# Performance work log

Measured on AMD Instinct MI355X. Metric: run time of the kernel, lower is better.

The kernel has to match this reference:

```python
import jax, jax.numpy as jnp
import numpy as np

N = 50000      # num nodes
DIN = 256
DOUT = 256
E = 400000     # edges per sign
NEG_SLOPE = 0.2  # LeakyReLU(0.2)


def setup_inputs() -> dict:
    key = jax.random.key(0)
    ks = jax.random.split(key, 12)
    p = lambda k, shp: jax.random.normal(k, shp, jnp.float32) * 0.05
    return {
        "node_reps": jax.random.normal(ks[0], (N, DIN), jnp.float32),
        "adj_pos": jax.random.randint(ks[1], (2, E), 0, N, dtype=jnp.int32),
        "adj_neg": jax.random.randint(ks[2], (2, E), 0, N, dtype=jnp.int32),
        "basis": p(ks[3], (2, DIN, DOUT)),        # num_bases=num_relations=2
        "att": p(ks[4], (2, 2)),
        "mapping_func": p(ks[5], (1, 2 * DOUT)),
        "bias": p(ks[6], (1, DOUT)),
        "theta1": p(ks[7], (DOUT, DOUT)),          # HGNN_conv 1 linear weight
        "b1": jnp.zeros((DOUT,), jnp.float32),
        "theta2": p(ks[8], (DOUT, DOUT)),          # HGNN_conv 2 linear weight
        "b2": jnp.zeros((DOUT,), jnp.float32),
    }


def reference(node_reps, adj_pos, adj_neg, basis, att, mapping_func, bias,
              theta1, b1, theta2, b2):
    # basis-decomposed relation weights: Wr[r] = sum_b att[r,b] * basis[b]
    Wr = (att @ basis.reshape(2, -1)).reshape(2, DIN, DOUT)
    h_pos = node_reps @ Wr[0]
    h_neg = node_reps @ Wr[1]
    # HGNN_conv feature transforms (linear + bias)
    h_pos = h_pos @ theta1 + b1
    h_neg = h_neg @ theta2 + b2

    # edge attention score: mapping_func . concat(h[src], h[dst])
    w_src = mapping_func[0, :DOUT]
    w_dst = mapping_func[0, DOUT:]
    e_pos = h_pos[adj_pos[0]] @ w_src + h_pos[adj_pos[1]] @ w_dst  # [E]
    e_neg = h_neg[adj_neg[0]] @ w_src + h_neg[adj_neg[1]] @ w_dst  # [E]
    e_all = jnp.concatenate([e_pos, e_neg])                         # [2E]
    coeff = jax.nn.sigmoid(jnp.where(e_all > 0, e_all, NEG_SLOPE * e_all))

    # symmetric degree normalization over the union graph
    rows_all = jnp.concatenate([adj_pos[0], adj_neg[0]])
    cols_all = jnp.concatenate([adj_pos[1], adj_neg[1]])
    deg = jnp.sqrt(jax.ops.segment_sum(
        jnp.ones_like(coeff), rows_all, num_segments=N))            # [N]
    coeff = coeff / (deg[rows_all] * deg[cols_all])

    # sparse aggregation (SpecialSpmm): out[r] += coeff_e * h[c]
    h_agg_pos = jax.ops.segment_sum(
        coeff[:E, None] * h_pos[adj_pos[1]], adj_pos[0], num_segments=N)
    h_agg_neg = jax.ops.segment_sum(
        coeff[E:, None] * h_neg[adj_neg[1]], adj_neg[0], num_segments=N)

    output = h_agg_pos - h_agg_neg + bias
    return (output, h_agg_pos, h_agg_neg)
```

## Files before the change

### kernel.cpp

```cpp
#include <hip/hip_runtime.h>

#define N_NODES 50000
#define NEDGE   400000
#define SB      512
#define NSB     ((N_NODES + SB - 1) / SB)
#define H8SCALE 128.0f

typedef __bf16 bf16x8 __attribute__((ext_vector_type(8)));
typedef float  f32x4  __attribute__((ext_vector_type(4)));
typedef float  f32x2  __attribute__((ext_vector_type(2)));
typedef unsigned short u16x8 __attribute__((ext_vector_type(8)));
typedef int    i32x2  __attribute__((ext_vector_type(2)));

#define GLDS16(gp, lp) \
  __builtin_amdgcn_global_load_lds((const __attribute__((address_space(1))) void*)(gp), \
                                   (__attribute__((address_space(3))) void*)(lp), 16, 0, 0)

static __device__ __forceinline__ unsigned short f2bf(float f) {
  unsigned u = __float_as_uint(f);
  unsigned r = (u + 0x7fffu + ((u >> 16) & 1u)) >> 16;
  return (unsigned short)r;
}
static __device__ __forceinline__ float bf2f(unsigned short v) {
  return __uint_as_float((unsigned)v << 16);
}

__global__ __launch_bounds__(256) void fused0_kernel(
    const float* __restrict__ basis, const float* __restrict__ att,
    const float* __restrict__ theta1, const float* __restrict__ theta2,
    const float* __restrict__ bias1, const float* __restrict__ bias2,
    unsigned short* __restrict__ Wt, float* __restrict__ biasvec,
    const float* __restrict__ node, unsigned short* __restrict__ A16,
    const int* __restrict__ adjp, const int* __restrict__ adjn,
    int* __restrict__ cntp, int* __restrict__ cntn) {
  const int b = blockIdx.x;
  if (b < 512) {
    const int r = b >> 8, k = b & 255;
    const int n = threadIdx.x;
    const float a0 = att[r * 2 + 0], a1 = att[r * 2 + 1];
    const float* th = (r == 0) ? theta1 : theta2;
    float acc = 0.f;
    for (int j = 0; j < 256; ++j) {
      const float wr = a0 * basis[k * 256 + j] + a1 * basis[65536 + k * 256 + j];
      acc += wr * th[j * 256 + n];
    }
    Wt[(size_t)(r * 256 + n) * 256 + k] = f2bf(acc);
    if (k == 0) biasvec[r * 256 + n] = (r == 0) ? bias1[n] : bias2[n];
  } else if (b < 2560) {
    const long total = (long)N_NODES * 256 / 4;
    long idx = (long)(b - 512) * 256 + threadIdx.x;
    const long stride = 2048L * 256;
    for (; idx < total; idx += stride) {
      const f32x4 v = __builtin_nontemporal_load(&((const f32x4*)node)[idx]);
      ushort4 o;
      o.x = f2bf(v.x); o.y = f2bf(v.y); o.z = f2bf(v.z); o.w = f2bf(v.w);
      ((ushort4*)A16)[idx] = o;
    }
  } else {
    const int g = (b - 2560) * 256 + threadIdx.x;
    if (g < NEDGE) atomicAdd(&cntp[adjp[g]], 1);
    else if (g < 2 * NEDGE) atomicAdd(&cntn[adjn[g - NEDGE]], 1);
  }
}

__global__ __launch_bounds__(256) void gemm_kernel(
    const unsigned short* __restrict__ A,
    const unsigned short* __restrict__ Wt,
    const float* __restrict__ biasvec,
    const float* __restrict__ mapping,
    unsigned char* __restrict__ H8,
    float* __restrict__ sdbuf) {
  __shared__ unsigned short smem[128 * 136];
  unsigned short* sA = smem;
  unsigned short* sB = smem + 8192;
  const int tid = threadIdx.x;
  const int wave = tid >> 6, lane = tid & 63;
  const int wm = wave >> 1, wn = wave & 1;
  const int m0 = blockIdx.y * 128;
  const int n0 = blockIdx.x * 128;

  f32x4 acc[4][4];
#pragma unroll
  for (int a = 0; a < 4; ++a)
#pragma unroll
    for (int b = 0; b < 4; ++b) acc[a][b] = (f32x4){0.f, 0.f, 0.f, 0.f};

  const int srow = lane >> 3;
  const int skel = ((lane & 7) ^ srow) << 3;

  for (int ks = 0; ks < 4; ++ks) {
    const int kg = ks * 64 + skel;
#pragma unroll
    for (int c = 0; c < 4; ++c) {
      const int chunk = wave * 4 + c;
      const int row = chunk * 8 + srow;
      int rowg = m0 + row;
      rowg = rowg < N_NODES ? rowg : N_NODES - 1;
      GLDS16(A + (size_t)rowg * 256 + kg, sA + chunk * 512);
      GLDS16(Wt + (size_t)(n0 + row) * 256 + kg, sB + chunk * 512);
    }
    __syncthreads();
#pragma unroll
    for (int kk = 0; kk < 2; ++kk) {
      const int kb = (kk * 32 + ((lane >> 4) << 3)) << 1;
      bf16x8 af[4], bfr[4];
#pragma unroll
      for (int m16 = 0; m16 < 4; ++m16) {
        const int row = wm * 64 + m16 * 16 + (lane & 15);
        af[m16] = *(const bf16x8*)((const char*)sA + row * 128 + (kb ^ ((row & 7) << 4)));
      }
#pragma unroll
      for (int n16 = 0; n16 < 4; ++n16) {
        const int col = wn * 64 + n16 * 16 + (lane & 15);
        bfr[n16] = *(const bf16x8*)((const char*)sB + col * 128 + (kb ^ ((col & 7) << 4)));
      }
#pragma unroll
      for (int m16 = 0; m16 < 4; ++m16)
#pragma unroll
        for (int n16 = 0; n16 < 4; ++n16)
          acc[m16][n16] = __builtin_amdgcn_mfma_f32_16x16x32_bf16(af[m16], bfr[n16], acc[m16][n16], 0, 0, 0);
    }
    __syncthreads();
  }

  const bool sgn = (n0 >= 256);
  const int nb = (sgn ? (n0 - 256) : n0) >> 7;
  const int slice = nb * 2 + wn;
  float* __restrict__ sS = sdbuf + ((size_t)((sgn ? 2 : 0) + 0) * 4 + slice) * N_NODES;
  float* __restrict__ sD = sdbuf + ((size_t)((sgn ? 2 : 0) + 1) * 4 + slice) * N_NODES;
  float bv[4], wsv[4], wdv[4];
#pragma unroll
  for (int n16 = 0; n16 < 4; ++n16) {
    const int colg = n0 + wn * 64 + n16 * 16 + (lane & 15);
    bv[n16] = biasvec[colg];
    const int cm = colg & 255;
    wsv[n16] = mapping[cm];
    wdv[n16] = mapping[256 + cm];
  }
#pragma unroll
  for (int m16 = 0; m16 < 4; ++m16) {
    const int rowb = wm * 64 + m16 * 16 + ((lane >> 4) << 2);
#pragma unroll
    for (int j = 0; j < 4; ++j) {
      const int rowl = rowb + j;
      float vs = 0.f, vd = 0.f;
#pragma unroll
      for (int n16 = 0; n16 < 4; ++n16) {
        const float v = acc[m16][n16][j] + bv[n16];
        const int coll = wn * 64 + n16 * 16 + (lane & 15);
        smem[rowl * 136 + coll] = f2bf(v);
        vs += v * wsv[n16];
        vd += v * wdv[n16];
      }
#pragma unroll
      for (int off = 1; off < 16; off <<= 1) { vs += __shfl_xor(vs, off); vd += __shfl_xor(vd, off); }
      const int rowg = m0 + rowl;
      if ((lane & 15) == 0 && rowg < N_NODES) { sS[rowg] = vs; sD[rowg] = vd; }
    }
  }
  __syncthreads();
#pragma unroll
  for (int it = 0; it < 8; ++it) {
    const int row = it * 16 + (tid >> 4);
    const int c8 = (tid & 15) * 8;
    const int rowg = m0 + row;
    if (rowg < N_NODES) {
      const u16x8 v = *(const u16x8*)(smem + row * 136 + c8);
      float f[8];
#pragma unroll
      for (int q = 0; q < 8; ++q) f[q] = bf2f((unsigned short)v[q]) * H8SCALE;
      int w0 = __builtin_amdgcn_cvt_pk_fp8_f32(f[0], f[1], 0, false);
      w0     = __builtin_amdgcn_cvt_pk_fp8_f32(f[2], f[3], w0, true);
      int w1 = __builtin_amdgcn_cvt_pk_fp8_f32(f[4], f[5], 0, false);
      w1     = __builtin_amdgcn_cvt_pk_fp8_f32(f[6], f[7], w1, true);
      i32x2 o; o.x = w0; o.y = w1;
      *(i32x2*)(&H8[(size_t)rowg * 512 + n0 + c8]) = o;
    }
  }
}

__global__ __launch_bounds__(SB) void scan1_kernel(const int* __restrict__ cntp,
                                                   const int* __restrict__ cntn,
                                                   int* __restrict__ bsp, int* __restrict__ bsn) {
  __shared__ int lp[SB / 64], ln[SB / 64];
  const int i = blockIdx.x * SB + threadIdx.x;
  int vp = (i < N_NODES) ? cntp[i] : 0;
  int vn = (i < N_NODES) ? cntn[i] : 0;
#pragma unroll
  for (int off = 1; off < 64; off <<= 1) { vp += __shfl_xor(vp, off); vn += __shfl_xor(vn, off); }
  const int wave = threadIdx.x >> 6, lane = threadIdx.x & 63;
  if (lane == 0) { lp[wave] = vp; ln[wave] = vn; }
  __syncthreads();
  if (threadIdx.x == 0) {
    int ap = 0, an = 0;
#pragma unroll
    for (int w = 0; w < SB / 64; ++w) { ap += lp[w]; an += ln[w]; }
    bsp[blockIdx.x] = ap; bsn[blockIdx.x] = an;
  }
}

__global__ void scan2_kernel(int* __restrict__ bsp, int* __restrict__ bsn,
                             int* __restrict__ rsp, int* __restrict__ rsn) {
  __shared__ int sp_[128], sn_[128];
  const int t = threadIdx.x;
  sp_[t] = (t < NSB) ? bsp[t] : 0;
  sn_[t] = (t < NSB) ? bsn[t] : 0;
  __syncthreads();
  for (int off = 1; off < 128; off <<= 1) {
    const int ap = (t >= off) ? sp_[t - off] : 0;
    const int an = (t >= off) ? sn_[t - off] : 0;
    __syncthreads();
    sp_[t] += ap; sn_[t] += an;
    __syncthreads();
  }
  if (t < NSB) { bsp[t] = (t == 0) ? 0 : sp_[t - 1]; bsn[t] = (t == 0) ? 0 : sn_[t - 1]; }
  if (t == 127) { rsp[N_NODES] = sp_[127]; rsn[N_NODES] = sn_[127]; }
}

__global__ __launch_bounds__(SB) void scan3_kernel(const int* __restrict__ cntp,
                                                   const int* __restrict__ cntn,
                                                   const int* __restrict__ bsp,
                                                   const int* __restrict__ bsn,
                                                   const float* __restrict__ sdbuf,
                                                   int* __restrict__ rsp, int* __restrict__ rsn,
                                                   int* __restrict__ curp, int* __restrict__ curn,
                                                   f32x4* __restrict__ nip, f32x4* __restrict__ nin) {
  __shared__ int sp_[SB], sn_[SB];
  const int t = threadIdx.x;
  const int i = blockIdx.x * SB + t;
  const int cp = (i < N_NODES) ? cntp[i] : 0;
  const int cn = (i < N_NODES) ? cntn[i] : 0;
  sp_[t] = cp; sn_[t] = cn;
  __syncthreads();
  for (int off = 1; off < SB; off <<= 1) {
    const int ap = (t >= off) ? sp_[t - off] : 0;
    const int an = (t >= off) ? sn_[t - off] : 0;
    __syncthreads();
    sp_[t] += ap; sn_[t] += an;
    __syncthreads();
  }
  if (i < N_NODES) {
    const int rp = bsp[blockIdx.x] + sp_[t] - cp;
    const int rn = bsn[blockIdx.x] + sn_[t] - cn;
    rsp[i] = rp; curp[i] = rp;
    rsn[i] = rn; curn[i] = rn;
    const float rdeg = 1.f / sqrtf((float)(cp + cn));
    float sp4 = 0.f, dp4 = 0.f, sn4 = 0.f, dn4 = 0.f;
#pragma unroll
    for (int sl = 0; sl < 4; ++sl) {
      sp4 += sdbuf[(size_t)(0 * 4 + sl) * N_NODES + i];
      dp4 += sdbuf[(size_t)(1 * 4 + sl) * N_NODES + i];
      sn4 += sdbuf[(size_t)(2 * 4 + sl) * N_NODES + i];
      dn4 += sdbuf[(size_t)(3 * 4 + sl) * N_NODES + i];
    }
    nip[i] = (f32x4){sp4, dp4, rdeg, 0.f};
    nin[i] = (f32x4){sn4, dn4, rdeg, 0.f};
  }
}

__global__ void scatter_kernel(const int* __restrict__ adjp, const int* __restrict__ adjn,
                               const f32x4* __restrict__ nip, const f32x4* __restrict__ nin,
                               int* __restrict__ curp, int* __restrict__ curn,
                               i32x2* __restrict__ ecp, i32x2* __restrict__ ecn) {
  const int g = blockIdx.x * blockDim.x + threadIdx.x;
  if (g >= 2 * NEDGE) return;
  const bool neg = (g >= NEDGE);
  const int e2 = neg ? g - NEDGE : g;
  const int* __restrict__ adj = neg ? adjn : adjp;
  const f32x4* __restrict__ ni = neg ? nin : nip;
  int* __restrict__ cur = neg ? curn : curp;
  i32x2* __restrict__ ec = neg ? ecn : ecp;
  const int src = adj[e2], dst = adj[NEDGE + e2];
  const f32x4 a = ni[src], b = ni[dst];
  const float e = a.x + b.y;
  const float l = e > 0.f ? e : 0.2f * e;
  const float c = (1.f / (1.f + expf(-l))) * a.z * b.z * (1.0f / H8SCALE);
  const int p = atomicAdd(&cur[src], 1);
  i32x2 w; w.x = dst; w.y = __float_as_int(c);
  ec[p] = w;
}

__global__ __launch_bounds__(256) void agg_kernel(
    const unsigned char* __restrict__ H8,
    const int* __restrict__ rsp, const i32x2* __restrict__ ecp,
    const int* __restrict__ rsn, const i32x2* __restrict__ ecn,
    const float* __restrict__ bias, float* __restrict__ out) {
  __shared__ f32x4 sneg[2][64];
  const int wave = threadIdx.x >> 6, lane = threadIdx.x & 63;
  const int r = wave >> 1;
  const int sign = wave & 1;
  const int i = blockIdx.x * 2 + r;
  const int* __restrict__ rs  = sign ? rsn : rsp;
  const i32x2* __restrict__ ec = sign ? ecn : ecp;
  const unsigned char* __restrict__ Hb = H8 + sign * 256 + (size_t)lane * 4;
  const int beg = rs[i], end = rs[i + 1];
  f32x4 a0 = {0,0,0,0}, a1 = {0,0,0,0}, a2 = {0,0,0,0}, a3 = {0,0,0,0};
  for (int chunk = beg; chunk < end; chunk += 64) {
    const int m = (end - chunk < 64) ? end - chunk : 64;
    i32x2 ev = {0, 0};
    if (lane < m) ev = __builtin_nontemporal_load(&ec[chunk + lane]);
    const int   cv = ev.x;
    const float fv = __int_as_float(ev.y);
    int k = 0;
    for (; k + 4 <= m; k += 4) {
      const int   c0 = __shfl(cv, k),     c1 = __shfl(cv, k + 1);
      const int   c2 = __shfl(cv, k + 2), c3 = __shfl(cv, k + 3);
      const float f0 = __shfl(fv, k),     f1 = __shfl(fv, k + 1);
      const float f2 = __shfl(fv, k + 2), f3 = __shfl(fv, k + 3);
      const unsigned w0 = *(const unsigned*)(Hb + (size_t)c0 * 512);
      const unsigned w1 = *(const unsigned*)(Hb + (size_t)c1 * 512);
      const unsigned w2 = *(const unsigned*)(Hb + (size_t)c2 * 512);
      const unsigned w3 = *(const unsigned*)(Hb + (size_t)c3 * 512);
      const f32x2 l0 = __builtin_amdgcn_cvt_pk_f32_fp8(w0, false), h0 = __builtin_amdgcn_cvt_pk_f32_fp8(w0, true);
      const f32x2 l1 = __builtin_amdgcn_cvt_pk_f32_fp8(w1, false), h1 = __builtin_amdgcn_cvt_pk_f32_fp8(w1, true);
      const f32x2 l2 = __builtin_amdgcn_cvt_pk_f32_fp8(w2, false), h2 = __builtin_amdgcn_cvt_pk_f32_fp8(w2, true);
      const f32x2 l3 = __builtin_amdgcn_cvt_pk_f32_fp8(w3, false), h3 = __builtin_amdgcn_cvt_pk_f32_fp8(w3, true);
      a0.x += f0 * l0.x; a0.y += f0 * l0.y; a0.z += f0 * h0.x; a0.w += f0 * h0.y;
      a1.x += f1 * l1.x; a1.y += f1 * l1.y; a1.z += f1 * h1.x; a1.w += f1 * h1.y;
      a2.x += f2 * l2.x; a2.y += f2 * l2.y; a2.z += f2 * h2.x; a2.w += f2 * h2.y;
      a3.x += f3 * l3.x; a3.y += f3 * l3.y; a3.z += f3 * h3.x; a3.w += f3 * h3.y;
    }
    for (; k < m; ++k) {
      const int   c0 = __shfl(cv, k);
      const float f0 = __shfl(fv, k);
      const unsigned w0 = *(const unsigned*)(Hb + (size_t)c0 * 512);
      const f32x2 l0 = __builtin_amdgcn_cvt_pk_f32_fp8(w0, false), h0 = __builtin_amdgcn_cvt_pk_f32_fp8(w0, true);
      a0.x += f0 * l0.x; a0.y += f0 * l0.y; a0.z += f0 * h0.x; a0.w += f0 * h0.y;
    }
  }
  f32x4 a = (a0 + a1) + (a2 + a3);
  if (sign) sneg[r][lane] = a;
  __syncthreads();
  if (sign) {
    __builtin_nontemporal_store(a, ((f32x4*)(out + (size_t)2 * N_NODES * 256)) + (size_t)i * 64 + lane);
  } else {
    const f32x4 an = sneg[r][lane];
    const f32x4 bv = ((const f32x4*)bias)[lane];
    const f32x4 o = a - an + bv;
    __builtin_nontemporal_store(o, ((f32x4*)out) + (size_t)i * 64 + lane);
    __builtin_nontemporal_store(a, ((f32x4*)(out + (size_t)N_NODES * 256)) + (size_t)i * 64 + lane);
  }
}

extern "C" void kernel_launch(void* const* d_in, const int* in_sizes, int n_in,
                              void* d_out, int out_size, void* d_ws, size_t ws_size,
                              hipStream_t stream) {
  const float* node    = (const float*)d_in[0];
  const int*   adjp    = (const int*)d_in[1];
  const int*   adjn    = (const int*)d_in[2];
  const float* basis   = (const float*)d_in[3];
  const float* att     = (const float*)d_in[4];
  const float* mapping = (const float*)d_in[5];
  const float* bias    = (const float*)d_in[6];
  const float* theta1  = (const float*)d_in[7];
  const float* b1      = (const float*)d_in[8];
  const float* theta2  = (const float*)d_in[9];
  const float* b2      = (const float*)d_in[10];
  float* out = (float*)d_out;

  size_t off = 0;
  char* wsb = (char*)d_ws;
  auto alloc = [&](size_t bytes) -> char* {
    char* p = wsb + off;
    off = (off + bytes + 255) & ~(size_t)255;
    return p;
  };
  unsigned short* A16 = (unsigned short*)alloc((size_t)N_NODES * 256 * 2);
  unsigned char*  H8  = (unsigned char*)alloc((size_t)N_NODES * 512);
  unsigned short* Wt  = (unsigned short*)alloc(512 * 256 * 2);
  float* biasvec = (float*)alloc(512 * 4);
  float* sdbuf = (float*)alloc((size_t)16 * N_NODES * 4);
  f32x4* nip = (f32x4*)alloc((size_t)N_NODES * 16);
  f32x4* nin = (f32x4*)alloc((size_t)N_NODES * 16);
  int* cnt2 = (int*)alloc((size_t)2 * N_NODES * 4);
  int* cntp = cnt2, *cntn = cnt2 + N_NODES;
  int* cur2 = (int*)alloc((size_t)2 * N_NODES * 4);
  int* curp = cur2, *curn = cur2 + N_NODES;
  int* rsp = (int*)alloc((N_NODES + 1) * 4);
  int* rsn = (int*)alloc((N_NODES + 1) * 4);
  int* bsp = (int*)alloc(NSB * 4);
  int* bsn = (int*)alloc(NSB * 4);
  i32x2* ecp = (i32x2*)alloc((size_t)NEDGE * 8);
  i32x2* ecn = (i32x2*)alloc((size_t)NEDGE * 8);

  (void)hipMemsetAsync(cnt2, 0, (size_t)2 * N_NODES * 4, stream);

  fused0_kernel<<<512 + 2048 + (2 * NEDGE) / 256, 256, 0, stream>>>(
      basis, att, theta1, theta2, b1, b2, Wt, biasvec, node, A16, adjp, adjn, cntp, cntn);
  gemm_kernel<<<dim3(4, 391), 256, 0, stream>>>(A16, Wt, biasvec, mapping, H8, sdbuf);
  scan1_kernel<<<NSB, SB, 0, stream>>>(cntp, cntn, bsp, bsn);
  scan2_kernel<<<1, 128, 0, stream>>>(bsp, bsn, rsp, rsn);
  scan3_kernel<<<NSB, SB, 0, stream>>>(cntp, cntn, bsp, bsn, sdbuf, rsp, rsn, curp, curn, nip, nin);
  scatter_kernel<<<(2 * NEDGE) / 256, 256, 0, stream>>>(adjp, adjn, nip, nin, curp, curn, ecp, ecn);
  agg_kernel<<<N_NODES / 2, 256, 0, stream>>>(H8, rsp, ecp, rsn, ecn, bias, out);
}
```

Before: 214.5 us.

## Fuse fp32-to-bf16 node conversion into GEMM and widen N tile to 256

```diff
diff --git a/kernel.cpp b/kernel.cpp
--- a/kernel.cpp
+++ b/kernel.cpp
@@ -21,8 +21,8 @@
   unsigned r = (u + 0x7fffu + ((u >> 16) & 1u)) >> 16;
   return (unsigned short)r;
 }
-static __device__ __forceinline__ float bf2f(unsigned short v) {
-  return __uint_as_float((unsigned)v << 16);
+static __device__ __forceinline__ unsigned char f2fp8(float f) {
+  return (unsigned char)(__builtin_amdgcn_cvt_pk_fp8_f32(f, f, 0, false) & 0xff);
 }
 
 __global__ __launch_bounds__(256) void fused0_kernel(
@@ -30,7 +30,6 @@
     const float* __restrict__ theta1, const float* __restrict__ theta2,
     const float* __restrict__ bias1, const float* __restrict__ bias2,
     unsigned short* __restrict__ Wt, float* __restrict__ biasvec,
-    const float* __restrict__ node, unsigned short* __restrict__ A16,
     const int* __restrict__ adjp, const int* __restrict__ adjn,
     int* __restrict__ cntp, int* __restrict__ cntn) {
   const int b = blockIdx.x;
@@ -46,92 +45,96 @@
     }
     Wt[(size_t)(r * 256 + n) * 256 + k] = f2bf(acc);
     if (k == 0) biasvec[r * 256 + n] = (r == 0) ? bias1[n] : bias2[n];
-  } else if (b < 2560) {
-    const long total = (long)N_NODES * 256 / 4;
-    long idx = (long)(b - 512) * 256 + threadIdx.x;
-    const long stride = 2048L * 256;
-    for (; idx < total; idx += stride) {
-      const f32x4 v = __builtin_nontemporal_load(&((const f32x4*)node)[idx]);
-      ushort4 o;
-      o.x = f2bf(v.x); o.y = f2bf(v.y); o.z = f2bf(v.z); o.w = f2bf(v.w);
-      ((ushort4*)A16)[idx] = o;
-    }
   } else {
-    const int g = (b - 2560) * 256 + threadIdx.x;
+    const int g = (b - 512) * 256 + threadIdx.x;
     if (g < NEDGE) atomicAdd(&cntp[adjp[g]], 1);
-    else if (g < 2 * NEDGE) atomicAdd(&cntn[adjn[g - NEDGE]], 1);
+    else           atomicAdd(&cntn[adjn[g - NEDGE]], 1);
   }
 }
 
 __global__ __launch_bounds__(256) void gemm_kernel(
-    const unsigned short* __restrict__ A,
+    const float* __restrict__ Af,
     const unsigned short* __restrict__ Wt,
     const float* __restrict__ biasvec,
     const float* __restrict__ mapping,
     unsigned char* __restrict__ H8,
     float* __restrict__ sdbuf) {
-  __shared__ unsigned short smem[128 * 136];
+  __shared__ unsigned short smem[24576];
   unsigned short* sA = smem;
   unsigned short* sB = smem + 8192;
   const int tid = threadIdx.x;
   const int wave = tid >> 6, lane = tid & 63;
   const int wm = wave >> 1, wn = wave & 1;
+  const int sgn = blockIdx.x;
   const int m0 = blockIdx.y * 128;
-  const int n0 = blockIdx.x * 128;
-
-  f32x4 acc[4][4];
+  const int n0 = sgn * 256;
+
+  f32x4 acc[4][8];
 #pragma unroll
   for (int a = 0; a < 4; ++a)
 #pragma unroll
-    for (int b = 0; b < 4; ++b) acc[a][b] = (f32x4){0.f, 0.f, 0.f, 0.f};
+    for (int b = 0; b < 8; ++b) acc[a][b] = (f32x4){0.f, 0.f, 0.f, 0.f};
 
   const int srow = lane >> 3;
   const int skel = ((lane & 7) ^ srow) << 3;
+  const int arow = tid >> 1;
+  const int akh  = (tid & 1) * 32;
+  int arowg = m0 + arow;
+  arowg = arowg < N_NODES ? arowg : N_NODES - 1;
+  const f32x4* asrc = (const f32x4*)(Af + (size_t)arowg * 256 + akh);
+  const int aswz = (arow & 7) << 4;
 
   for (int ks = 0; ks < 4; ++ks) {
     const int kg = ks * 64 + skel;
 #pragma unroll
-    for (int c = 0; c < 4; ++c) {
-      const int chunk = wave * 4 + c;
-      const int row = chunk * 8 + srow;
-      int rowg = m0 + row;
-      rowg = rowg < N_NODES ? rowg : N_NODES - 1;
-      GLDS16(A + (size_t)rowg * 256 + kg, sA + chunk * 512);
-      GLDS16(Wt + (size_t)(n0 + row) * 256 + kg, sB + chunk * 512);
+    for (int c = 0; c < 8; ++c) {
+      const int chunk = wave * 8 + c;
+      const int brow = chunk * 8 + srow;
+      GLDS16(Wt + (size_t)(n0 + brow) * 256 + kg, sB + chunk * 512);
+    }
+    {
+      const f32x4* src = asrc + ks * 16;
+#pragma unroll
+      for (int c = 0; c < 4; ++c) {
+        const f32x4 v0 = src[c * 2], v1 = src[c * 2 + 1];
+        u16x8 hv;
+        hv[0] = f2bf(v0.x); hv[1] = f2bf(v0.y); hv[2] = f2bf(v0.z); hv[3] = f2bf(v0.w);
+        hv[4] = f2bf(v1.x); hv[5] = f2bf(v1.y); hv[6] = f2bf(v1.z); hv[7] = f2bf(v1.w);
+        const int boff = arow * 128 + ((akh * 2 + c * 16) ^ aswz);
+        *(u16x8*)((char*)sA + boff) = hv;
+      }
     }
     __syncthreads();
 #pragma unroll
     for (int kk = 0; kk < 2; ++kk) {
       const int kb = (kk * 32 + ((lane >> 4) << 3)) << 1;
-      bf16x8 af[4], bfr[4];
+      bf16x8 af[4], bfr[8];
 #pragma unroll
       for (int m16 = 0; m16 < 4; ++m16) {
         const int row = wm * 64 + m16 * 16 + (lane & 15);
         af[m16] = *(const bf16x8*)((const char*)sA + row * 128 + (kb ^ ((row & 7) << 4)));
       }
 #pragma unroll
-      for (int n16 = 0; n16 < 4; ++n16) {
-        const int col = wn * 64 + n16 * 16 + (lane & 15);
+      for (int n16 = 0; n16 < 8; ++n16) {
+        const int col = wn * 128 + n16 * 16 + (lane & 15);
         bfr[n16] = *(const bf16x8*)((const char*)sB + col * 128 + (kb ^ ((col & 7) << 4)));
       }
 #pragma unroll
       for (int m16 = 0; m16 < 4; ++m16)
 #pragma unroll
-        for (int n16 = 0; n16 < 4; ++n16)
+        for (int n16 = 0; n16 < 8; ++n16)
           acc[m16][n16] = __builtin_amdgcn_mfma_f32_16x16x32_bf16(af[m16], bfr[n16], acc[m16][n16], 0, 0, 0);
     }
     __syncthreads();
   }
 
-  const bool sgn = (n0 >= 256);
-  const int nb = (sgn ? (n0 - 256) : n0) >> 7;
-  const int slice = nb * 2 + wn;
-  float* __restrict__ sS = sdbuf + ((size_t)((sgn ? 2 : 0) + 0) * 4 + slice) * N_NODES;
-  float* __restrict__ sD = sdbuf + ((size_t)((sgn ? 2 : 0) + 1) * 4 + slice) * N_NODES;
-  float bv[4], wsv[4], wdv[4];
-#pragma unroll
-  for (int n16 = 0; n16 < 4; ++n16) {
-    const int colg = n0 + wn * 64 + n16 * 16 + (lane & 15);
+  unsigned char* smem8 = (unsigned char*)smem;
+  float* __restrict__ sS = sdbuf + ((size_t)((sgn * 2 + 0) * 2 + wn)) * N_NODES;
+  float* __restrict__ sD = sdbuf + ((size_t)((sgn * 2 + 1) * 2 + wn)) * N_NODES;
+  float bv[8], wsv[8], wdv[8];
+#pragma unroll
+  for (int n16 = 0; n16 < 8; ++n16) {
+    const int colg = n0 + wn * 128 + n16 * 16 + (lane & 15);
     bv[n16] = biasvec[colg];
     const int cm = colg & 255;
     wsv[n16] = mapping[cm];
@@ -145,10 +148,10 @@
       const int rowl = rowb + j;
       float vs = 0.f, vd = 0.f;
 #pragma unroll
-      for (int n16 = 0; n16 < 4; ++n16) {
+      for (int n16 = 0; n16 < 8; ++n16) {
         const float v = acc[m16][n16][j] + bv[n16];
-        const int coll = wn * 64 + n16 * 16 + (lane & 15);
-        smem[rowl * 136 + coll] = f2bf(v);
+        const int coll = wn * 128 + n16 * 16 + (lane & 15);
+        smem8[rowl * 272 + coll] = f2fp8(v * H8SCALE);
         vs += v * wsv[n16];
         vd += v * wdv[n16];
       }
@@ -159,22 +162,14 @@
     }
   }
   __syncthreads();
-#pragma unroll
-  for (int it = 0; it < 8; ++it) {
-    const int row = it * 16 + (tid >> 4);
-    const int c8 = (tid & 15) * 8;
+  {
+    const int row = tid >> 1, half = tid & 1;
     const int rowg = m0 + row;
     if (rowg < N_NODES) {
-      const u16x8 v = *(const u16x8*)(smem + row * 136 + c8);
-      float f[8];
-#pragma unroll
-      for (int q = 0; q < 8; ++q) f[q] = bf2f((unsigned short)v[q]) * H8SCALE;
-      int w0 = __builtin_amdgcn_cvt_pk_fp8_f32(f[0], f[1], 0, false);
-      w0     = __builtin_amdgcn_cvt_pk_fp8_f32(f[2], f[3], w0, true);
-      int w1 = __builtin_amdgcn_cvt_pk_fp8_f32(f[4], f[5], 0, false);
-      w1     = __builtin_amdgcn_cvt_pk_fp8_f32(f[6], f[7], w1, true);
-      i32x2 o; o.x = w0; o.y = w1;
-      *(i32x2*)(&H8[(size_t)rowg * 512 + n0 + c8]) = o;
+      const f32x4* s = (const f32x4*)(smem8 + row * 272 + half * 128);
+      f32x4* d = (f32x4*)(H8 + (size_t)rowg * 512 + n0 + half * 128);
+#pragma unroll
+      for (int c = 0; c < 8; ++c) d[c] = s[c];
     }
   }
 }
@@ -245,14 +240,10 @@
     rsp[i] = rp; curp[i] = rp;
     rsn[i] = rn; curn[i] = rn;
     const float rdeg = 1.f / sqrtf((float)(cp + cn));
-    float sp4 = 0.f, dp4 = 0.f, sn4 = 0.f, dn4 = 0.f;
-#pragma unroll
-    for (int sl = 0; sl < 4; ++sl) {
-      sp4 += sdbuf[(size_t)(0 * 4 + sl) * N_NODES + i];
-      dp4 += sdbuf[(size_t)(1 * 4 + sl) * N_NODES + i];
-      sn4 += sdbuf[(size_t)(2 * 4 + sl) * N_NODES + i];
-      dn4 += sdbuf[(size_t)(3 * 4 + sl) * N_NODES + i];
-    }
+    const float sp4 = sdbuf[(size_t)0 * N_NODES + i] + sdbuf[(size_t)1 * N_NODES + i];
+    const float dp4 = sdbuf[(size_t)2 * N_NODES + i] + sdbuf[(size_t)3 * N_NODES + i];
+    const float sn4 = sdbuf[(size_t)4 * N_NODES + i] + sdbuf[(size_t)5 * N_NODES + i];
+    const float dn4 = sdbuf[(size_t)6 * N_NODES + i] + sdbuf[(size_t)7 * N_NODES + i];
     nip[i] = (f32x4){sp4, dp4, rdeg, 0.f};
     nin[i] = (f32x4){sn4, dn4, rdeg, 0.f};
   }
@@ -295,6 +286,16 @@
   const unsigned char* __restrict__ Hb = H8 + sign * 256 + (size_t)lane * 4;
   const int beg = rs[i], end = rs[i + 1];
   f32x4 a0 = {0,0,0,0}, a1 = {0,0,0,0}, a2 = {0,0,0,0}, a3 = {0,0,0,0};
+  f32x4 a4 = {0,0,0,0}, a5 = {0,0,0,0}, a6 = {0,0,0,0}, a7 = {0,0,0,0};
+#define GSTEP(ACC, KOFF)                                                              \
+  {                                                                                   \
+    const int   c_ = __shfl(cv, k + (KOFF));                                          \
+    const float f_ = __shfl(fv, k + (KOFF));                                          \
+    const unsigned w_ = *(const unsigned*)(Hb + (size_t)c_ * 512);                    \
+    const f32x2 lo_ = __builtin_amdgcn_cvt_pk_f32_fp8(w_, false);                     \
+    const f32x2 hi_ = __builtin_amdgcn_cvt_pk_f32_fp8(w_, true);                      \
+    ACC.x += f_ * lo_.x; ACC.y += f_ * lo_.y; ACC.z += f_ * hi_.x; ACC.w += f_ * hi_.y; \
+  }
   for (int chunk = beg; chunk < end; chunk += 64) {
     const int m = (end - chunk < 64) ? end - chunk : 64;
     i32x2 ev = {0, 0};
@@ -302,33 +303,14 @@
     const int   cv = ev.x;
     const float fv = __int_as_float(ev.y);
     int k = 0;
-    for (; k + 4 <= m; k += 4) {
-      const int   c0 = __shfl(cv, k),     c1 = __shfl(cv, k + 1);
-      const int   c2 = __shfl(cv, k + 2), c3 = __shfl(cv, k + 3);
-      const float f0 = __shfl(fv, k),     f1 = __shfl(fv, k + 1);
-      const float f2 = __shfl(fv, k + 2), f3 = __shfl(fv, k + 3);
-      const unsigned w0 = *(const unsigned*)(Hb + (size_t)c0 * 512);
-      const unsigned w1 = *(const unsigned*)(Hb + (size_t)c1 * 512);
-      const unsigned w2 = *(const unsigned*)(Hb + (size_t)c2 * 512);
-      const unsigned w3 = *(const unsigned*)(Hb + (size_t)c3 * 512);
-      const f32x2 l0 = __builtin_amdgcn_cvt_pk_f32_fp8(w0, false), h0 = __builtin_amdgcn_cvt_pk_f32_fp8(w0, true);
-      const f32x2 l1 = __builtin_amdgcn_cvt_pk_f32_fp8(w1, false), h1 = __builtin_amdgcn_cvt_pk_f32_fp8(w1, true);
-      const f32x2 l2 = __builtin_amdgcn_cvt_pk_f32_fp8(w2, false), h2 = __builtin_amdgcn_cvt_pk_f32_fp8(w2, true);
-      const f32x2 l3 = __builtin_amdgcn_cvt_pk_f32_fp8(w3, false), h3 = __builtin_amdgcn_cvt_pk_f32_fp8(w3, true);
-      a0.x += f0 * l0.x; a0.y += f0 * l0.y; a0.z += f0 * h0.x; a0.w += f0 * h0.y;
-      a1.x += f1 * l1.x; a1.y += f1 * l1.y; a1.z += f1 * h1.x; a1.w += f1 * h1.y;
-      a2.x += f2 * l2.x; a2.y += f2 * l2.y; a2.z += f2 * h2.x; a2.w += f2 * h2.y;
-      a3.x += f3 * l3.x; a3.y += f3 * l3.y; a3.z += f3 * h3.x; a3.w += f3 * h3.y;
-    }
-    for (; k < m; ++k) {
-      const int   c0 = __shfl(cv, k);
-      const float f0 = __shfl(fv, k);
-      const unsigned w0 = *(const unsigned*)(Hb + (size_t)c0 * 512);
-      const f32x2 l0 = __builtin_amdgcn_cvt_pk_f32_fp8(w0, false), h0 = __builtin_amdgcn_cvt_pk_f32_fp8(w0, true);
-      a0.x += f0 * l0.x; a0.y += f0 * l0.y; a0.z += f0 * h0.x; a0.w += f0 * h0.y;
-    }
-  }
-  f32x4 a = (a0 + a1) + (a2 + a3);
+    for (; k + 8 <= m; k += 8) {
+      GSTEP(a0, 0) GSTEP(a1, 1) GSTEP(a2, 2) GSTEP(a3, 3)
+      GSTEP(a4, 4) GSTEP(a5, 5) GSTEP(a6, 6) GSTEP(a7, 7)
+    }
+    for (; k < m; ++k) GSTEP(a0, 0)
+  }
+#undef GSTEP
+  f32x4 a = ((a0 + a1) + (a2 + a3)) + ((a4 + a5) + (a6 + a7));
   if (sign) sneg[r][lane] = a;
   __syncthreads();
   if (sign) {
@@ -365,11 +347,10 @@
     off = (off + bytes + 255) & ~(size_t)255;
     return p;
   };
-  unsigned short* A16 = (unsigned short*)alloc((size_t)N_NODES * 256 * 2);
   unsigned char*  H8  = (unsigned char*)alloc((size_t)N_NODES * 512);
   unsigned short* Wt  = (unsigned short*)alloc(512 * 256 * 2);
   float* biasvec = (float*)alloc(512 * 4);
-  float* sdbuf = (float*)alloc((size_t)16 * N_NODES * 4);
+  float* sdbuf = (float*)alloc((size_t)8 * N_NODES * 4);
   f32x4* nip = (f32x4*)alloc((size_t)N_NODES * 16);
   f32x4* nin = (f32x4*)alloc((size_t)N_NODES * 16);
   int* cnt2 = (int*)alloc((size_t)2 * N_NODES * 4);
@@ -385,9 +366,9 @@
 
   (void)hipMemsetAsync(cnt2, 0, (size_t)2 * N_NODES * 4, stream);
 
-  fused0_kernel<<<512 + 2048 + (2 * NEDGE) / 256, 256, 0, stream>>>(
-      basis, att, theta1, theta2, b1, b2, Wt, biasvec, node, A16, adjp, adjn, cntp, cntn);
-  gemm_kernel<<<dim3(4, 391), 256, 0, stream>>>(A16, Wt, biasvec, mapping, H8, sdbuf);
+  fused0_kernel<<<512 + (2 * NEDGE) / 256, 256, 0, stream>>>(
+      basis, att, theta1, theta2, b1, b2, Wt, biasvec, adjp, adjn, cntp, cntn);
+  gemm_kernel<<<dim3(2, 391), 256, 0, stream>>>(node, Wt, biasvec, mapping, H8, sdbuf);
   scan1_kernel<<<NSB, SB, 0, stream>>>(cntp, cntn, bsp, bsn);
   scan2_kernel<<<1, 128, 0, stream>>>(bsp, bsn, rsp, rsn);
   scan3_kernel<<<NSB, SB, 0, stream>>>(cntp, cntn, bsp, bsn, sdbuf, rsp, rsn, curp, curn, nip, nin);
```

Result: slower. 270.4 us (+26.0%).

## Map 16-lane groups per edge with 16-byte fp8 row loads in aggregation

Applied to the files above, without the earlier changes.

```diff
diff --git a/kernel.cpp b/kernel.cpp
--- a/kernel.cpp
+++ b/kernel.cpp
@@ -11,6 +11,7 @@
 typedef float  f32x2  __attribute__((ext_vector_type(2)));
 typedef unsigned short u16x8 __attribute__((ext_vector_type(8)));
 typedef int    i32x2  __attribute__((ext_vector_type(2)));
+typedef unsigned int u32x4 __attribute__((ext_vector_type(4)));
 
 #define GLDS16(gp, lp) \
   __builtin_amdgcn_global_load_lds((const __attribute__((address_space(1))) void*)(gp), \
@@ -23,6 +24,12 @@
 }
 static __device__ __forceinline__ float bf2f(unsigned short v) {
   return __uint_as_float((unsigned)v << 16);
+}
+static __device__ __forceinline__ f32x4 shflxor4(f32x4 v, int m) {
+  f32x4 r;
+  r.x = __shfl_xor(v.x, m); r.y = __shfl_xor(v.y, m);
+  r.z = __shfl_xor(v.z, m); r.w = __shfl_xor(v.w, m);
+  return r;
 }
 
 __global__ __launch_bounds__(256) void fused0_kernel(
@@ -285,60 +292,63 @@
     const int* __restrict__ rsp, const i32x2* __restrict__ ecp,
     const int* __restrict__ rsn, const i32x2* __restrict__ ecn,
     const float* __restrict__ bias, float* __restrict__ out) {
-  __shared__ f32x4 sneg[2][64];
+  __shared__ float sneg[2][256];
   const int wave = threadIdx.x >> 6, lane = threadIdx.x & 63;
   const int r = wave >> 1;
   const int sign = wave & 1;
   const int i = blockIdx.x * 2 + r;
   const int* __restrict__ rs  = sign ? rsn : rsp;
   const i32x2* __restrict__ ec = sign ? ecn : ecp;
-  const unsigned char* __restrict__ Hb = H8 + sign * 256 + (size_t)lane * 4;
+  const int g16 = lane >> 4;
+  const int l16 = lane & 15;
+  const unsigned char* __restrict__ Hb = H8 + sign * 256 + l16 * 16;
   const int beg = rs[i], end = rs[i + 1];
-  f32x4 a0 = {0,0,0,0}, a1 = {0,0,0,0}, a2 = {0,0,0,0}, a3 = {0,0,0,0};
+  f32x4 A0 = {0,0,0,0}, A1 = {0,0,0,0}, A2 = {0,0,0,0}, A3 = {0,0,0,0};
+#define DECW(W, ACC)                                                                  \
+  {                                                                                   \
+    const f32x2 lo_ = __builtin_amdgcn_cvt_pk_f32_fp8((W), false);                    \
+    const f32x2 hi_ = __builtin_amdgcn_cvt_pk_f32_fp8((W), true);                     \
+    ACC.x += f_ * lo_.x; ACC.y += f_ * lo_.y; ACC.z += f_ * hi_.x; ACC.w += f_ * hi_.y; \
+  }
   for (int chunk = beg; chunk < end; chunk += 64) {
     const int m = (end - chunk < 64) ? end - chunk : 64;
     i32x2 ev = {0, 0};
     if (lane < m) ev = __builtin_nontemporal_load(&ec[chunk + lane]);
     const int   cv = ev.x;
     const float fv = __int_as_float(ev.y);
-    int k = 0;
-    for (; k + 4 <= m; k += 4) {
-      const int   c0 = __shfl(cv, k),     c1 = __shfl(cv, k + 1);
-      const int   c2 = __shfl(cv, k + 2), c3 = __shfl(cv, k + 3);
-      const float f0 = __shfl(fv, k),     f1 = __shfl(fv, k + 1);
-      const float f2 = __shfl(fv, k + 2), f3 = __shfl(fv, k + 3);
-      const unsigned w0 = *(const unsigned*)(Hb + (size_t)c0 * 512);
-      const unsigned w1 = *(const unsigned*)(Hb + (size_t)c1 * 512);
-      const unsigned w2 = *(const unsigned*)(Hb + (size_t)c2 * 512);
-      const unsigned w3 = *(const unsigned*)(Hb + (size_t)c3 * 512);
-      const f32x2 l0 = __builtin_amdgcn_cvt_pk_f32_fp8(w0, false), h0 = __builtin_amdgcn_cvt_pk_f32_fp8(w0, true);
-      const f32x2 l1 = __builtin_amdgcn_cvt_pk_f32_fp8(w1, false), h1 = __builtin_amdgcn_cvt_pk_f32_fp8(w1, true);
-      const f32x2 l2 = __builtin_amdgcn_cvt_pk_f32_fp8(w2, false), h2 = __builtin_amdgcn_cvt_pk_f32_fp8(w2, true);
-      const f32x2 l3 = __builtin_amdgcn_cvt_pk_f32_fp8(w3, false), h3 = __builtin_amdgcn_cvt_pk_f32_fp8(w3, true);
-      a0.x += f0 * l0.x; a0.y += f0 * l0.y; a0.z += f0 * h0.x; a0.w += f0 * h0.y;
-      a1.x += f1 * l1.x; a1.y += f1 * l1.y; a1.z += f1 * h1.x; a1.w += f1 * h1.y;
-      a2.x += f2 * l2.x; a2.y += f2 * l2.y; a2.z += f2 * h2.x; a2.w += f2 * h2.y;
-      a3.x += f3 * l3.x; a3.y += f3 * l3.y; a3.z += f3 * h3.x; a3.w += f3 * h3.y;
-    }
-    for (; k < m; ++k) {
-      const int   c0 = __shfl(cv, k);
-      const float f0 = __shfl(fv, k);
-      const unsigned w0 = *(const unsigned*)(Hb + (size_t)c0 * 512);
-      const f32x2 l0 = __builtin_amdgcn_cvt_pk_f32_fp8(w0, false), h0 = __builtin_amdgcn_cvt_pk_f32_fp8(w0, true);
-      a0.x += f0 * l0.x; a0.y += f0 * l0.y; a0.z += f0 * h0.x; a0.w += f0 * h0.y;
-    }
-  }
-  f32x4 a = (a0 + a1) + (a2 + a3);
-  if (sign) sneg[r][lane] = a;
+    for (int k = 0; k < m; k += 4) {
+      const int e = k + g16;
+      const int   c_ = __shfl(cv, e);
+      const float f_ = __shfl(fv, e);
+      const u32x4 w = *(const u32x4*)(Hb + (size_t)c_ * 512);
+      DECW(w[0], A0) DECW(w[1], A1) DECW(w[2], A2) DECW(w[3], A3)
+    }
+  }
+#undef DECW
+  A0 += shflxor4(A0, 16); A1 += shflxor4(A1, 16); A2 += shflxor4(A2, 16); A3 += shflxor4(A3, 16);
+  A0 += shflxor4(A0, 32); A1 += shflxor4(A1, 32); A2 += shflxor4(A2, 32); A3 += shflxor4(A3, 32);
+  if (sign && lane < 16) {
+    f32x4* s = (f32x4*)&sneg[r][l16 * 16];
+    s[0] = A0; s[1] = A1; s[2] = A2; s[3] = A3;
+  }
   __syncthreads();
-  if (sign) {
-    __builtin_nontemporal_store(a, ((f32x4*)(out + (size_t)2 * N_NODES * 256)) + (size_t)i * 64 + lane);
-  } else {
-    const f32x4 an = sneg[r][lane];
-    const f32x4 bv = ((const f32x4*)bias)[lane];
-    const f32x4 o = a - an + bv;
-    __builtin_nontemporal_store(o, ((f32x4*)out) + (size_t)i * 64 + lane);
-    __builtin_nontemporal_store(a, ((f32x4*)(out + (size_t)N_NODES * 256)) + (size_t)i * 64 + lane);
+  if (lane < 16) {
+    if (sign) {
+      f32x4* d = ((f32x4*)(out + (size_t)2 * N_NODES * 256 + (size_t)i * 256)) + l16 * 4;
+      __builtin_nontemporal_store(A0, d + 0); __builtin_nontemporal_store(A1, d + 1);
+      __builtin_nontemporal_store(A2, d + 2); __builtin_nontemporal_store(A3, d + 3);
+    } else {
+      const f32x4* an = (const f32x4*)&sneg[r][l16 * 16];
+      const f32x4* bv = ((const f32x4*)bias) + l16 * 4;
+      f32x4* dp = ((f32x4*)(out + (size_t)N_NODES * 256 + (size_t)i * 256)) + l16 * 4;
+      f32x4* dо = ((f32x4*)(out + (size_t)i * 256)) + l16 * 4;
+      __builtin_nontemporal_store(A0, dp + 0); __builtin_nontemporal_store(A1, dp + 1);
+      __builtin_nontemporal_store(A2, dp + 2); __builtin_nontemporal_store(A3, dp + 3);
+      const f32x4 o0 = A0 - an[0] + bv[0], o1 = A1 - an[1] + bv[1];
+      const f32x4 o2 = A2 - an[2] + bv[2], o3 = A3 - an[3] + bv[3];
+      __builtin_nontemporal_store(o0, dо + 0); __builtin_nontemporal_store(o1, dо + 1);
+      __builtin_nontemporal_store(o2, dо + 2); __builtin_nontemporal_store(o3, dо + 3);
+    }
   }
 }
 
```

Result: slower. 222.5 us (+3.7%).

## Fold block-sum scan into scan3 and unroll weight-fusion loop

Applied to the files above, without the earlier changes.

```diff
diff --git a/kernel.cpp b/kernel.cpp
--- a/kernel.cpp
+++ b/kernel.cpp
@@ -39,12 +39,20 @@
     const int n = threadIdx.x;
     const float a0 = att[r * 2 + 0], a1 = att[r * 2 + 1];
     const float* th = (r == 0) ? theta1 : theta2;
-    float acc = 0.f;
-    for (int j = 0; j < 256; ++j) {
-      const float wr = a0 * basis[k * 256 + j] + a1 * basis[65536 + k * 256 + j];
-      acc += wr * th[j * 256 + n];
-    }
-    Wt[(size_t)(r * 256 + n) * 256 + k] = f2bf(acc);
+    const float* b0 = basis + k * 256;
+    const float* b1p = basis + 65536 + k * 256;
+    float ac0 = 0.f, ac1 = 0.f, ac2 = 0.f, ac3 = 0.f;
+    for (int j = 0; j < 256; j += 4) {
+      const float w0 = a0 * b0[j + 0] + a1 * b1p[j + 0];
+      const float w1 = a0 * b0[j + 1] + a1 * b1p[j + 1];
+      const float w2 = a0 * b0[j + 2] + a1 * b1p[j + 2];
+      const float w3 = a0 * b0[j + 3] + a1 * b1p[j + 3];
+      ac0 += w0 * th[(j + 0) * 256 + n];
+      ac1 += w1 * th[(j + 1) * 256 + n];
+      ac2 += w2 * th[(j + 2) * 256 + n];
+      ac3 += w3 * th[(j + 3) * 256 + n];
+    }
+    Wt[(size_t)(r * 256 + n) * 256 + k] = f2bf((ac0 + ac1) + (ac2 + ac3));
     if (k == 0) biasvec[r * 256 + n] = (r == 0) ? bias1[n] : bias2[n];
   } else if (b < 2560) {
     const long total = (long)N_NODES * 256 / 4;
@@ -199,24 +207,6 @@
   }
 }
 
-__global__ void scan2_kernel(int* __restrict__ bsp, int* __restrict__ bsn,
-                             int* __restrict__ rsp, int* __restrict__ rsn) {
-  __shared__ int sp_[128], sn_[128];
-  const int t = threadIdx.x;
-  sp_[t] = (t < NSB) ? bsp[t] : 0;
-  sn_[t] = (t < NSB) ? bsn[t] : 0;
-  __syncthreads();
-  for (int off = 1; off < 128; off <<= 1) {
-    const int ap = (t >= off) ? sp_[t - off] : 0;
-    const int an = (t >= off) ? sn_[t - off] : 0;
-    __syncthreads();
-    sp_[t] += ap; sn_[t] += an;
-    __syncthreads();
-  }
-  if (t < NSB) { bsp[t] = (t == 0) ? 0 : sp_[t - 1]; bsn[t] = (t == 0) ? 0 : sn_[t - 1]; }
-  if (t == 127) { rsp[N_NODES] = sp_[127]; rsn[N_NODES] = sn_[127]; }
-}
-
 __global__ __launch_bounds__(SB) void scan3_kernel(const int* __restrict__ cntp,
                                                    const int* __restrict__ cntn,
                                                    const int* __restrict__ bsp,
@@ -226,7 +216,24 @@
                                                    int* __restrict__ curp, int* __restrict__ curn,
                                                    f32x4* __restrict__ nip, f32x4* __restrict__ nin) {
   __shared__ int sp_[SB], sn_[SB];
+  __shared__ int pbs[128], nbs[128];
   const int t = threadIdx.x;
+  if (t < 128) {
+    pbs[t] = (t < NSB) ? bsp[t] : 0;
+    nbs[t] = (t < NSB) ? bsn[t] : 0;
+  }
+  __syncthreads();
+  for (int off = 1; off < 128; off <<= 1) {
+    const int ap = (t >= off && t < 128) ? pbs[t - off] : 0;
+    const int an = (t >= off && t < 128) ? nbs[t - off] : 0;
+    __syncthreads();
+    if (t < 128) { pbs[t] += ap; nbs[t] += an; }
+    __syncthreads();
+  }
+  const int basep = (blockIdx.x == 0) ? 0 : pbs[blockIdx.x - 1];
+  const int basen = (blockIdx.x == 0) ? 0 : nbs[blockIdx.x - 1];
+  if (blockIdx.x == 0 && t == 0) { rsp[N_NODES] = pbs[127]; rsn[N_NODES] = nbs[127]; }
+
   const int i = blockIdx.x * SB + t;
   const int cp = (i < N_NODES) ? cntp[i] : 0;
   const int cn = (i < N_NODES) ? cntn[i] : 0;
@@ -240,8 +247,8 @@
     __syncthreads();
   }
   if (i < N_NODES) {
-    const int rp = bsp[blockIdx.x] + sp_[t] - cp;
-    const int rn = bsn[blockIdx.x] + sn_[t] - cn;
+    const int rp = basep + sp_[t] - cp;
+    const int rn = basen + sn_[t] - cn;
     rsp[i] = rp; curp[i] = rp;
     rsn[i] = rn; curn[i] = rn;
     const float rdeg = 1.f / sqrtf((float)(cp + cn));
@@ -389,7 +396,6 @@
       basis, att, theta1, theta2, b1, b2, Wt, biasvec, node, A16, adjp, adjn, cntp, cntn);
   gemm_kernel<<<dim3(4, 391), 256, 0, stream>>>(A16, Wt, biasvec, mapping, H8, sdbuf);
   scan1_kernel<<<NSB, SB, 0, stream>>>(cntp, cntn, bsp, bsn);
-  scan2_kernel<<<1, 128, 0, stream>>>(bsp, bsn, rsp, rsn);
   scan3_kernel<<<NSB, SB, 0, stream>>>(cntp, cntn, bsp, bsn, sdbuf, rsp, rsn, curp, curn, nip, nin);
   scatter_kernel<<<(2 * NEDGE) / 256, 256, 0, stream>>>(adjp, adjn, nip, nin, curp, curn, ecp, ecn);
   agg_kernel<<<N_NODES / 2, 256, 0, stream>>>(H8, rsp, ecp, rsn, ecn, bias, out);
```

After: 210.8 us (median of 2 runs). About the same (-1.7%).
